# Performance work log

Measured on AMD Instinct MI355X. Metric: run time of the kernel, lower is better.

Reference implementation:

```python
import jax, jax.numpy as jnp
import numpy as np

D_MODEL, D_STATE, D_CONV, EXPAND = 1024, 16, 4, 2
D_INNER = EXPAND * D_MODEL
DT_RANK = D_MODEL // 16
B, T = 2, 4096
EPS = 1e-5


def setup_inputs() -> dict:
    key = jax.random.key(0)
    ks = jax.random.split(key, 8)
    s = lambda k, shape, sc: jax.random.normal(k, shape, jnp.float32) * sc
    return {
        "x": s(ks[0], (B, T, D_MODEL), 1.0),
        "norm_w": jnp.ones((D_MODEL,), jnp.float32),
        "w_in": s(ks[1], (D_MODEL, 2 * D_INNER), 0.02),
        "conv_w": s(ks[2], (D_INNER, 1, D_CONV), 0.1),   # depthwise kernel (O,I/g,K)
        "conv_b": jnp.zeros((D_INNER,), jnp.float32),
        "w_x": s(ks[3], (D_INNER, DT_RANK + 2 * D_STATE), 0.02),
        "w_dt": s(ks[4], (DT_RANK, D_INNER), 0.02),
        "b_dt": s(ks[5], (D_INNER,), 0.02),
        "A_log": jnp.log(jnp.broadcast_to(
            jnp.arange(1, D_STATE + 1, dtype=jnp.float32), (D_INNER, D_STATE))),
        "D": jnp.ones((D_INNER,), jnp.float32),
        "w_out": s(ks[6], (D_INNER, D_MODEL), 0.02),
    }


def _rmsnorm(x, w):
    return x * jax.lax.rsqrt(jnp.mean(x * x, axis=-1, keepdims=True) + EPS) * w


def _mamba(x, w_in, conv_w, conv_b, w_x, w_dt, b_dt, A_log, Dp, w_out):
    xr = x @ w_in                                  # (B,T,2*D_INNER)
    u, res = jnp.split(xr, 2, axis=-1)
    # causal depthwise conv over time
    uc = jnp.transpose(u, (0, 2, 1))               # (B,D_INNER,T)
    uc = jax.lax.conv_general_dilated(
        uc, conv_w, window_strides=(1,), padding=[(D_CONV - 1, 0)],
        dimension_numbers=("NCH", "OIH", "NCH"), feature_group_count=D_INNER)
    u = jax.nn.silu(jnp.transpose(uc, (0, 2, 1)) + conv_b)  # (B,T,D_INNER)

    xdbc = u @ w_x                                 # (B,T,DT_RANK+2*D_STATE)
    dt, Bm, Cm = jnp.split(xdbc, [DT_RANK, DT_RANK + D_STATE], axis=-1)
    delta = jax.nn.softplus(dt @ w_dt + b_dt)      # (B,T,D_INNER)
    A = -jnp.exp(A_log)                            # (D_INNER,D_STATE)

    def step(h, inp):
        d_t, b_t, c_t, u_t = inp                   # (B,Di),(B,N),(B,N),(B,Di)
        dA = jnp.exp(d_t[:, :, None] * A)          # (B,Di,N)
        h = dA * h + (d_t * u_t)[:, :, None] * b_t[:, None, :]
        y_t = jnp.einsum("bdn,bn->bd", h, c_t)
        return h, y_t

    h0 = jnp.zeros((x.shape[0], D_INNER, D_STATE), x.dtype)
    xs = (jnp.swapaxes(delta, 0, 1), jnp.swapaxes(Bm, 0, 1),
          jnp.swapaxes(Cm, 0, 1), jnp.swapaxes(u, 0, 1))
    _, ys = jax.lax.scan(step, h0, xs)             # ys: (T,B,D_INNER)
    y = jnp.swapaxes(ys, 0, 1) + u * Dp            # (B,T,D_INNER)
    y = y * jax.nn.silu(res)
    return y @ w_out                               # (B,T,D_MODEL)


def reference(x, norm_w, w_in, conv_w, conv_b, w_x, w_dt, b_dt, A_log, D, w_out):
    return x + _mamba(_rmsnorm(x, norm_w), w_in, conv_w, conv_b,
                      w_x, w_dt, b_dt, A_log, D, w_out)
```

## Files before the change

### kernel.cpp

```cpp
#include <hip/hip_runtime.h>
#include <hip/hip_bf16.h>
#include <cmath>

typedef __hip_bfloat16 bf16;
typedef __attribute__((ext_vector_type(8))) short short8;
typedef __attribute__((ext_vector_type(4))) short short4v;
typedef __attribute__((ext_vector_type(4))) float floatx4;
typedef __attribute__((ext_vector_type(2))) float floatx2;
typedef __attribute__((ext_vector_type(4))) int intx4;

#define DMODEL 1024
#define DSTATE 16
#define DINNER 2048
#define DTRANK 64
#define NB 2
#define NT 4096
#define NM (NB * NT)
#define GG (2 * DINNER)
#define CL 64
#define NC (NT / CL)
#define LOG2E 1.4426950408889634f

typedef __attribute__((address_space(1))) const void gvoid;
typedef __attribute__((address_space(3))) void lvoid;
static __device__ __forceinline__ void gl_lds16(const bf16* g, bf16* l) {
  __builtin_amdgcn_global_load_lds((gvoid*)g, (lvoid*)l, 16, 0, 0);
}
static __device__ __forceinline__ void gl_lds16b(const void* g, void* l) {
  __builtin_amdgcn_global_load_lds((gvoid*)g, (lvoid*)l, 16, 0, 0);
}

static __device__ __forceinline__ float bits2f(unsigned short s) {
  unsigned u = ((unsigned)s) << 16;
  float f;
  __builtin_memcpy(&f, &u, 4);
  return f;
}
static __device__ __forceinline__ short f2bits(float f) {
  bf16 h = __float2bfloat16(f);
  short s;
  __builtin_memcpy(&s, &h, 2);
  return s;
}

__global__ void detect_k(const void* __restrict__ a_log_raw, int* __restrict__ flag,
                         int* __restrict__ sflag) {
  int lane = threadIdx.x;
  unsigned first = ((const unsigned*)a_log_raw)[0];
  int fl = (first != 0u) ? 1 : 0;
  int n = lane & 15;
  int grp = lane >> 4;
  int dsel = (grp == 0) ? 0 : (grp == 1) ? 1 : (grp == 2) ? 777 : 2047;
  int idx = dsel * DSTATE + n;
  float v = fl ? bits2f(((const unsigned short*)a_log_raw)[idx])
               : ((const float*)a_log_raw)[idx];
  float a = __expf(v);
  float tgt = (float)(n + 1);
  bool ok2 = fabsf(a - tgt) < 1e-5f * tgt;
  bool ok1 = fabsf(a - tgt) < 1.5e-2f * tgt;
  unsigned long long m2 = __ballot(ok2);
  unsigned long long m1 = __ballot(ok1);
  if (lane == 0) {
    *flag = fl;
    *sflag = (m2 == ~0ull) ? 2 : (m1 == ~0ull) ? 1 : 0;
  }
}

static __device__ __forceinline__ bf16 cvt1(const void* in, int i, int fl) {
  return fl ? ((const bf16*)in)[i] : __float2bfloat16(((const float*)in)[i]);
}
__global__ void convert_small_k(
    const void* nw, const void* cw, const void* cb, const void* bdt,
    const void* al, const void* dp, bf16* nwb, bf16* cwb, bf16* cbb, bf16* bdtb,
    bf16* alogb, bf16* Db, const int* __restrict__ flag) {
  int i = blockIdx.x * 256 + threadIdx.x;
  int fl = *flag;
  if (i < 1024) { nwb[i] = cvt1(nw, i, fl); return; } i -= 1024;
  if (i < 8192) { cwb[i] = cvt1(cw, i, fl); return; } i -= 8192;
  if (i < 2048) { cbb[i] = cvt1(cb, i, fl); return; } i -= 2048;
  if (i < 2048) { bdtb[i] = cvt1(bdt, i, fl); return; } i -= 2048;
  if (i < 32768) { alogb[i] = cvt1(al, i, fl); return; } i -= 32768;
  if (i < 2048) { Db[i] = cvt1(dp, i, fl); }
}

__global__ void transpose_k(const void* __restrict__ in, bf16* __restrict__ out,
                            int R, int C, const int* __restrict__ flag) {
  size_t idx = (size_t)blockIdx.x * 256 + threadIdx.x;
  if (idx >= (size_t)R * C) return;
  int fl = *flag;
  int c = (int)(idx / R);
  int r = (int)(idx % R);
  size_t src = (size_t)r * C + c;
  bf16 v = fl ? ((const bf16*)in)[src] : __float2bfloat16(((const float*)in)[src]);
  out[(size_t)c * R + r] = v;
}

__global__ __launch_bounds__(256) void transpose_tile_k(
    const void* __restrict__ in, bf16* __restrict__ out, int R, int C,
    const int* __restrict__ flag) {
  __shared__ bf16 t[64][65];
  int c0 = blockIdx.x * 64, r0 = blockIdx.y * 64;
  int fl = *flag;
  int ci = threadIdx.x & 63, grp = threadIdx.x >> 6;
#pragma unroll
  for (int rr = grp; rr < 64; rr += 4) {
    size_t src = (size_t)(r0 + rr) * C + c0 + ci;
    t[rr][ci] = fl ? ((const bf16*)in)[src]
                   : __float2bfloat16(((const float*)in)[src]);
  }
  __syncthreads();
#pragma unroll
  for (int cc = grp; cc < 64; cc += 4) {
    out[(size_t)(c0 + cc) * R + r0 + ci] = t[ci][cc];
  }
}

__global__ __launch_bounds__(256) void rmsnorm_k(const void* __restrict__ x,
                                                 const bf16* __restrict__ w,
                                                 bf16* __restrict__ xn,
                                                 const int* __restrict__ flag) {
  int row = blockIdx.x;
  int tid = threadIdx.x;
  int fl = *flag;
  float f[4];
  if (fl) {
    short4v raw = *(const short4v*)((const bf16*)x + (size_t)row * DMODEL + tid * 4);
#pragma unroll
    for (int k = 0; k < 4; k++) f[k] = bits2f((unsigned short)raw[k]);
  } else {
    floatx4 raw = *(const floatx4*)((const float*)x + (size_t)row * DMODEL + tid * 4);
#pragma unroll
    for (int k = 0; k < 4; k++) f[k] = raw[k];
  }
  float s = f[0] * f[0] + f[1] * f[1] + f[2] * f[2] + f[3] * f[3];
#pragma unroll
  for (int o = 32; o > 0; o >>= 1) s += __shfl_down(s, o);
  __shared__ float ps[4];
  __shared__ float stot;
  if ((tid & 63) == 0) ps[tid >> 6] = s;
  __syncthreads();
  if (tid == 0) stot = ps[0] + ps[1] + ps[2] + ps[3];
  __syncthreads();
  float scale = 1.0f / sqrtf(stot * (1.0f / DMODEL) + 1e-5f);
  short4v wr = *(const short4v*)(w + tid * 4);
  short4v o;
#pragma unroll
  for (int k = 0; k < 4; k++)
    o[k] = f2bits(f[k] * scale * bits2f((unsigned short)wr[k]));
  *(short4v*)(xn + (size_t)row * DMODEL + tid * 4) = o;
}

template <int EPI, int MT>
__global__ __launch_bounds__(256, 2) void gemm_bt(
    const bf16* __restrict__ A, const bf16* __restrict__ Bt, void* __restrict__ Cout,
    int M, int N, int K, int Ks, const bf16* __restrict__ eb,
    const void* __restrict__ ex, bf16* __restrict__ dtb,
    const int* __restrict__ flag) {
  constexpr int AI = MT / 32;
  constexpr bool COEPI = (EPI == 0 || EPI == 2 || EPI == 3 || EPI == 5);
  constexpr int AB_BYTES = (MT * 32 + 128 * 32) * 2;
  constexpr int ET_BYTES = COEPI ? 32 * 132 * 4 : 0;
  constexpr int SM_BYTES = AB_BYTES > ET_BYTES ? AB_BYTES : ET_BYTES;
  __shared__ __align__(16) char smraw[SM_BYTES];
  bf16* As = (bf16*)smraw;
  bf16* Bs = (bf16*)smraw + MT * 32;
  float* ET = (float*)smraw;

  int tid = threadIdx.x;
  int lane = tid & 63;
  int wave = tid >> 6;
  int wm = (wave >> 1) * (MT / 2), wn = (wave & 1) * 64;
  int m0 = blockIdx.y * MT, n0 = blockIdx.x * 128;
  int koff = (EPI == 4) ? blockIdx.z * K : 0;

  floatx4 acc[AI][4] = {};

  int sr = tid >> 2;
  int sc = (tid & 3) * 8;
  int bn0 = n0 + sr;        if (bn0 > N - 1) bn0 = N - 1;
  int bn1 = n0 + sr + 64;   if (bn1 > N - 1) bn1 = N - 1;
  bf16* asb = As + wave * 512;
  bf16* bsb = Bs + wave * 512;

  const bf16* a0p = A + (size_t)(m0 + sr) * Ks + sc + koff;
  const bf16* a1p = A + (size_t)(m0 + sr + (MT == 128 ? 64 : 0)) * Ks + sc + koff;
  const bf16* b0p = Bt + (size_t)bn0 * Ks + sc + koff;
  const bf16* b1p = Bt + (size_t)bn1 * Ks + sc + koff;

  for (int k0 = 0; k0 < K; k0 += 32) {
    __syncthreads();
    gl_lds16(a0p + k0, asb);
    if (MT == 128) gl_lds16(a1p + k0, asb + 64 * 32);
    gl_lds16(b0p + k0, bsb);
    gl_lds16(b1p + k0, bsb + 64 * 32);
    __syncthreads();

    int fr = lane & 15;
    int q = lane >> 4;
    short8 af[AI], bfr[4];
#pragma unroll
    for (int i = 0; i < AI; i++)
      af[i] = *(const short8*)(As + (wm + i * 16 + fr) * 32 + q * 8);
#pragma unroll
    for (int j = 0; j < 4; j++)
      bfr[j] = *(const short8*)(Bs + (wn + j * 16 + fr) * 32 + q * 8);
#pragma unroll
    for (int i = 0; i < AI; i++)
#pragma unroll
      for (int j = 0; j < 4; j++)
        acc[i][j] =
            __builtin_amdgcn_mfma_f32_16x16x32_bf16(af[i], bfr[j], acc[i][j], 0, 0, 0);
  }

  int cr = (lane >> 4) * 4;
  int cc = lane & 15;

  if constexpr (COEPI) {
    int fl = (EPI == 3) ? *flag : 0;
    bool sil = (EPI == 5) && (n0 >= DINNER);
    int lrb = (wave >> 1) * 16 + cr;
    int r2 = tid >> 3;
#pragma unroll
    for (int i = 0; i < AI; i++) {
      __syncthreads();
#pragma unroll
      for (int j = 0; j < 4; j++)
#pragma unroll
        for (int r = 0; r < 4; r++)
          ET[(lrb + r) * 132 + wn + j * 16 + cc] = acc[i][j][r];
      __syncthreads();
      int m = m0 + i * 16 + (r2 < 16 ? r2 : r2 + 48);
      size_t rowo = (size_t)m * N + n0;
      if constexpr (EPI == 0 || EPI == 5) {
#pragma unroll
        for (int c = 0; c < 2; c++) {
          int col = (tid & 7) * 8 + c * 64;
          floatx4 f0 = *(const floatx4*)&ET[r2 * 132 + col];
          floatx4 f1 = *(const floatx4*)&ET[r2 * 132 + col + 4];
          short8 o8;
#pragma unroll
          for (int k = 0; k < 4; k++) {
            float v0 = f0[k], v1 = f1[k];
            if (EPI == 5 && sil) {
              v0 = v0 / (1.f + __expf(-v0));
              v1 = v1 / (1.f + __expf(-v1));
            }
            o8[k] = f2bits(v0);
            o8[4 + k] = f2bits(v1);
          }
          *(short8*)((bf16*)Cout + rowo + col) = o8;
        }
      } else if constexpr (EPI == 2) {
#pragma unroll
        for (int c = 0; c < 4; c++) {
          int col = (tid & 7) * 4 + c * 32;
          floatx4 f = *(const floatx4*)&ET[r2 * 132 + col];
          short4v eb4 = *(const short4v*)(eb + n0 + col);
          floatx4 o;
#pragma unroll
          for (int k = 0; k < 4; k++) {
            float t = f[k] + bits2f((unsigned short)eb4[k]);
            o[k] = (t > 15.f) ? t : __logf(1.f + __expf(t));
          }
          *(floatx4*)((float*)Cout + rowo + col) = o;
        }
      } else {
#pragma unroll
        for (int c = 0; c < 4; c++) {
          int col = (tid & 7) * 4 + c * 32;
          floatx4 f = *(const floatx4*)&ET[r2 * 132 + col];
          if (fl) {
            short4v xv = *(const short4v*)((const bf16*)ex + rowo + col);
            short4v o;
#pragma unroll
            for (int k = 0; k < 4; k++)
              o[k] = f2bits(f[k] + bits2f((unsigned short)xv[k]));
            *(short4v*)((bf16*)Cout + rowo + col) = o;
          } else {
            floatx4 xv = *(const floatx4*)((const float*)ex + rowo + col);
            floatx4 o;
#pragma unroll
            for (int k = 0; k < 4; k++) o[k] = f[k] + xv[k];
            *(floatx4*)((float*)Cout + rowo + col) = o;
          }
        }
      }
    }
  } else {
#pragma unroll
    for (int i = 0; i < AI; i++) {
#pragma unroll
      for (int j = 0; j < 4; j++) {
        int n = n0 + wn + j * 16 + cc;
        if (n >= N) continue;
#pragma unroll
        for (int r = 0; r < 4; r++) {
          int m = m0 + wm + i * 16 + cr + r;
          float v = acc[i][j][r];
          size_t o = (size_t)m * N + n;
          if (EPI == 1) {
            ((float*)Cout)[o] = v;
            if (n < DTRANK) dtb[(size_t)m * DTRANK + n] = __float2bfloat16(v);
          } else {
            ((float*)Cout)[((size_t)blockIdx.z * M + m) * N + n] = v;
          }
        }
      }
    }
  }
}

__global__ void reduce_dt_k(const float* __restrict__ part, float* __restrict__ xdbc,
                            bf16* __restrict__ dtb) {
  int idx = blockIdx.x * 256 + threadIdx.x;
  const int seg = NM * 96;
  float s = part[idx] + part[seg + idx] + part[2 * seg + idx] + part[3 * seg + idx];
  xdbc[idx] = s;
  int m = idx / 96, n = idx - m * 96;
  if (n < DTRANK) dtb[m * DTRANK + n] = __float2bfloat16(s);
}

__global__ __launch_bounds__(256) void conv_silu_k(const bf16* __restrict__ xr,
                                                   const bf16* __restrict__ cw,
                                                   const bf16* __restrict__ cb,
                                                   bf16* __restrict__ u) {
  size_t i8 = ((size_t)blockIdx.x * 256 + threadIdx.x) * 8;
  int col = (int)(i8 & (DINNER - 1));
  size_t m = i8 >> 11;
  int t = (int)(m & (NT - 1));
  float wv[8][4];
  {
    short8 w01 = *(const short8*)(cw + col * 4);
    short8 w23 = *(const short8*)(cw + col * 4 + 8);
    short8 w45 = *(const short8*)(cw + col * 4 + 16);
    short8 w67 = *(const short8*)(cw + col * 4 + 24);
#pragma unroll
    for (int j = 0; j < 4; j++) {
      wv[0][j] = bits2f((unsigned short)w01[j]);
      wv[1][j] = bits2f((unsigned short)w01[4 + j]);
      wv[2][j] = bits2f((unsigned short)w23[j]);
      wv[3][j] = bits2f((unsigned short)w23[4 + j]);
      wv[4][j] = bits2f((unsigned short)w45[j]);
      wv[5][j] = bits2f((unsigned short)w45[4 + j]);
      wv[6][j] = bits2f((unsigned short)w67[j]);
      wv[7][j] = bits2f((unsigned short)w67[4 + j]);
    }
  }
  short8 bias = *(const short8*)(cb + col);
  short8 rows[4] = {};
  const bf16* baseT = xr + m * GG + col;
  if (t >= 3) {
#pragma unroll
    for (int j = 0; j < 4; j++)
      rows[j] = *(const short8*)(baseT + (ptrdiff_t)(j - 3) * GG);
  } else {
    for (int j = 3 - t; j < 4; j++)
      rows[j] = *(const short8*)(baseT + (ptrdiff_t)(j - 3) * GG);
  }
  short8 outv;
#pragma unroll
  for (int i = 0; i < 8; i++) {
    float acc = bits2f((unsigned short)bias[i]);
#pragma unroll
    for (int j = 0; j < 4; j++)
      acc = fmaf(wv[i][j], bits2f((unsigned short)rows[j][i]), acc);
    float s = acc / (1.f + __expf(-acc));
    outv[i] = f2bits(s);
  }
  *(short8*)(u + m * DINNER + col) = outv;
}


template <int SM>
static __device__ __forceinline__ void scan1_impl(
    float* __restrict__ smB,
    const float* __restrict__ delta, const bf16* __restrict__ u,
    const float* __restrict__ xdbc, const bf16* __restrict__ A_log,
    float* __restrict__ chunkSd, float* __restrict__ chunkS) {
  int tid = threadIdx.x;
  int bc = blockIdx.x;
  int dblk = bc & 7;
  int chunk = (bc >> 3) & (NC - 1);
  int b = bc >> 9;
  int d = (dblk << 8) + tid;
  size_t base = (size_t)b * NT + (size_t)chunk * CL;

  {
    int byte = tid * 16;
    int t = byte >> 6;
    gl_lds16b((const char*)xdbc + (base + t) * 384 + 256 + (byte & 63),
              (char*)smB + byte);
  }

  const floatx2 one2 = {1.f, 1.f};
  float AvL[16];
  floatx2 rc2[8];
  if (SM == 0) {
#pragma unroll
    for (int k = 0; k < 16; k++)
      AvL[k] = -__expf((float)A_log[d * DSTATE + k]) * LOG2E;
  } else if (SM == 1) {
#pragma unroll
    for (int p = 0; p < 8; p++) {
      rc2[p][0] = __expf((float)A_log[d * DSTATE + 2 * p]) - (float)(2 * p + 1);
      rc2[p][1] = __expf((float)A_log[d * DSTATE + 2 * p + 1]) - (float)(2 * p + 2);
    }
  }

  const float* pd = delta + base * DINNER + d;
  const bf16* pu = u + base * DINNER + d;

  floatx2 h2[8] = {};
  float sd = 0.f;

  auto body = [&](float dlc, float uuc, int t) {
    float du = dlc * uuc;
    sd += dlc;
    floatx2 du2 = {du, du};
    const floatx4* bq = (const floatx4*)&smB[t * 16];
    floatx4 b0 = bq[0], b1 = bq[1], b2 = bq[2], b3 = bq[3];
    floatx2 B2[8] = {{b0[0], b0[1]}, {b0[2], b0[3]}, {b1[0], b1[1]}, {b1[2], b1[3]},
                     {b2[0], b2[1]}, {b2[2], b2[3]}, {b3[0], b3[1]}, {b3[2], b3[3]}};
    if (SM >= 1) {
      float e0 = exp2f(dlc * -LOG2E);
      float e2 = e0 * e0;
      floatx2 dv = {e0, e2};
      floatx2 e2v = {e2, e2};
      floatx2 mdl2 = {-dlc, -dlc};
#pragma unroll
      for (int p = 0; p < 8; p++) {
        floatx2 cA2 = dv;
        if (SM == 1)
          cA2 = dv * __builtin_elementwise_fma(mdl2, rc2[p], one2);
        h2[p] = __builtin_elementwise_fma(cA2, h2[p], du2 * B2[p]);
        dv *= e2v;
      }
    } else {
#pragma unroll
      for (int p = 0; p < 8; p++) {
        floatx2 cA2 = {exp2f(dlc * AvL[2 * p]), exp2f(dlc * AvL[2 * p + 1])};
        h2[p] = __builtin_elementwise_fma(cA2, h2[p], du2 * B2[p]);
      }
    }
  };

  float dlA = *pd, uuA = (float)*pu;
  pd += DINNER; pu += DINNER;
  __syncthreads();
  float dlB, uuB;
  for (int t = 0; t + 2 < CL; t += 2) {
    dlB = *pd; uuB = (float)*pu;
    pd += DINNER; pu += DINNER;
    body(dlA, uuA, t);
    dlA = *pd; uuA = (float)*pu;
    pd += DINNER; pu += DINNER;
    body(dlB, uuB, t + 1);
  }
  dlB = *pd; uuB = (float)*pu;
  body(dlA, uuA, CL - 2);
  body(dlB, uuB, CL - 1);

  size_t cidx = ((size_t)b * NC + chunk) * DINNER + d;
  float* out = chunkS + cidx * DSTATE;
  floatx4 S0 = {h2[0][0], h2[0][1], h2[1][0], h2[1][1]};
  floatx4 S1 = {h2[2][0], h2[2][1], h2[3][0], h2[3][1]};
  floatx4 S2 = {h2[4][0], h2[4][1], h2[5][0], h2[5][1]};
  floatx4 S3 = {h2[6][0], h2[6][1], h2[7][0], h2[7][1]};
  *(floatx4*)(out) = S0;
  *(floatx4*)(out + 4) = S1;
  *(floatx4*)(out + 8) = S2;
  *(floatx4*)(out + 12) = S3;
  chunkSd[cidx] = sd;
}

__global__ __launch_bounds__(256) void scan1_k(
    const float* __restrict__ delta, const bf16* __restrict__ u,
    const float* __restrict__ xdbc, const bf16* __restrict__ A_log,
    float* __restrict__ chunkSd, float* __restrict__ chunkS,
    const int* __restrict__ sflag) {
  __shared__ float smB[CL * 16];
  int sm = *sflag;
  if (sm == 2)      scan1_impl<2>(smB, delta, u, xdbc, A_log, chunkSd, chunkS);
  else if (sm == 1) scan1_impl<1>(smB, delta, u, xdbc, A_log, chunkSd, chunkS);
  else              scan1_impl<0>(smB, delta, u, xdbc, A_log, chunkSd, chunkS);
}

__global__ __launch_bounds__(256) void scan2_k(
    const float* __restrict__ chunkSd, const float* __restrict__ chunkS,
    const bf16* __restrict__ A_log, float* __restrict__ chunkH) {
  int tid = threadIdx.x;
  int bc = blockIdx.x;
  int dblk = bc & 31;
  int b = bc >> 5;
  int d = (dblk << 6) + (tid >> 2);
  int n0 = (tid & 3) * 4;
  float AvL[4];
#pragma unroll
  for (int k = 0; k < 4; k++)
    AvL[k] = -__expf((float)A_log[d * DSTATE + n0 + k]) * LOG2E;
  floatx4 h = {};
  size_t c0 = (size_t)b * NC * DINNER + d;
  size_t o0 = c0 * DSTATE + n0;
  floatx4 S = *(const floatx4*)(chunkS + o0);
  float sd = chunkSd[c0];
  for (int c = 0; c < NC; c++) {
    floatx4 Sn = {};
    float sd_n = 0.f;
    if (c + 1 < NC) {
      size_t cn = c0 + (size_t)(c + 1) * DINNER;
      Sn = *(const floatx4*)(chunkS + cn * DSTATE + n0);
      sd_n = chunkSd[cn];
    }
    size_t o = o0 + (size_t)c * DINNER * DSTATE;
    *(floatx4*)(chunkH + o) = h;
#pragma unroll
    for (int k = 0; k < 4; k++) h[k] = fmaf(exp2f(AvL[k] * sd), h[k], S[k]);
    S = Sn; sd = sd_n;
  }
}

template <int SM>
static __device__ __forceinline__ void scan3_impl(
    float* __restrict__ smBC,
    const float* __restrict__ delta, const bf16* __restrict__ u,
    const float* __restrict__ xdbc, const bf16* __restrict__ xr,
    const bf16* __restrict__ A_log, const bf16* __restrict__ Dp,
    const float* __restrict__ chunkH, bf16* __restrict__ y) {
  int tid = threadIdx.x;
  int bc = blockIdx.x;
  int dblk = bc & 7;
  int chunk = (bc >> 3) & (NC - 1);
  int b = bc >> 9;
  int d = (dblk << 8) + tid;
  size_t base = (size_t)b * NT + (size_t)chunk * CL;

#pragma unroll
  for (int j = 0; j < 2; j++) {
    int byte = (tid + 256 * j) * 16;
    int t = byte >> 7;
    gl_lds16b((const char*)xdbc + (base + t) * 384 + 256 + (byte & 127),
              (char*)smBC + byte);
  }

  const floatx2 one2 = {1.f, 1.f};
  float AvL[16];
  floatx2 rc2[8];
  if (SM == 0) {
#pragma unroll
    for (int k = 0; k < 16; k++)
      AvL[k] = -__expf((float)A_log[d * DSTATE + k]) * LOG2E;
  } else if (SM == 1) {
#pragma unroll
    for (int p = 0; p < 8; p++) {
      rc2[p][0] = __expf((float)A_log[d * DSTATE + 2 * p]) - (float)(2 * p + 1);
      rc2[p][1] = __expf((float)A_log[d * DSTATE + 2 * p + 1]) - (float)(2 * p + 2);
    }
  }
  float Dd = (float)Dp[d];
  floatx2 h2[8];
  {
    const float* hp = chunkH + (((size_t)b * NC + chunk) * DINNER + d) * DSTATE;
    floatx4 H0 = *(const floatx4*)(hp);
    floatx4 H1 = *(const floatx4*)(hp + 4);
    floatx4 H2 = *(const floatx4*)(hp + 8);
    floatx4 H3 = *(const floatx4*)(hp + 12);
    h2[0] = {H0[0], H0[1]}; h2[1] = {H0[2], H0[3]};
    h2[2] = {H1[0], H1[1]}; h2[3] = {H1[2], H1[3]};
    h2[4] = {H2[0], H2[1]}; h2[5] = {H2[2], H2[3]};
    h2[6] = {H3[0], H3[1]}; h2[7] = {H3[2], H3[3]};
  }

  const float* pd = delta + base * DINNER + d;
  const bf16* pu = u + base * DINNER + d;
  const bf16* pg = xr + base * GG + DINNER + d;
  bf16* py = y + base * DINNER + d;

  auto body = [&](float dlc, float uuc, float gfc, int t) {
    float du = dlc * uuc;
    floatx2 du2 = {du, du};
    const floatx4* bq = (const floatx4*)&smBC[t * 32];
    floatx4 b0 = bq[0], b1 = bq[1], b2 = bq[2], b3 = bq[3];
    floatx4 c0 = bq[4], c1 = bq[5], c2 = bq[6], c3 = bq[7];
    floatx2 B2[8] = {{b0[0], b0[1]}, {b0[2], b0[3]}, {b1[0], b1[1]}, {b1[2], b1[3]},
                     {b2[0], b2[1]}, {b2[2], b2[3]}, {b3[0], b3[1]}, {b3[2], b3[3]}};
    floatx2 C2[8] = {{c0[0], c0[1]}, {c0[2], c0[3]}, {c1[0], c1[1]}, {c1[2], c1[3]},
                     {c2[0], c2[1]}, {c2[2], c2[3]}, {c3[0], c3[1]}, {c3[2], c3[3]}};
    floatx2 ys2 = {0.f, 0.f};
    if (SM >= 1) {
      float e0 = exp2f(dlc * -LOG2E);
      float e2 = e0 * e0;
      floatx2 dv = {e0, e2};
      floatx2 e2v = {e2, e2};
      floatx2 mdl2 = {-dlc, -dlc};
#pragma unroll
      for (int p = 0; p < 8; p++) {
        floatx2 cA2 = dv;
        if (SM == 1)
          cA2 = dv * __builtin_elementwise_fma(mdl2, rc2[p], one2);
        h2[p] = __builtin_elementwise_fma(cA2, h2[p], du2 * B2[p]);
        ys2 = __builtin_elementwise_fma(h2[p], C2[p], ys2);
        dv *= e2v;
      }
    } else {
#pragma unroll
      for (int p = 0; p < 8; p++) {
        floatx2 cA2 = {exp2f(dlc * AvL[2 * p]), exp2f(dlc * AvL[2 * p + 1])};
        h2[p] = __builtin_elementwise_fma(cA2, h2[p], du2 * B2[p]);
        ys2 = __builtin_elementwise_fma(h2[p], C2[p], ys2);
      }
    }
    float ys = ys2[0] + ys2[1];
    *py = __float2bfloat16((ys + uuc * Dd) * gfc);
    py += DINNER;
  };

  float dlA = *pd, uuA = (float)*pu, gfA = (float)*pg;
  pd += DINNER; pu += DINNER; pg += GG;
  __syncthreads();
  float dlB, uuB, gfB;
  for (int t = 0; t + 2 < CL; t += 2) {
    dlB = *pd; uuB = (float)*pu; gfB = (float)*pg;
    pd += DINNER; pu += DINNER; pg += GG;
    body(dlA, uuA, gfA, t);
    dlA = *pd; uuA = (float)*pu; gfA = (float)*pg;
    pd += DINNER; pu += DINNER; pg += GG;
    body(dlB, uuB, gfB, t + 1);
  }
  dlB = *pd; uuB = (float)*pu; gfB = (float)*pg;
  body(dlA, uuA, gfA, CL - 2);
  body(dlB, uuB, gfB, CL - 1);
}

__global__ __launch_bounds__(256) void scan3_k(
    const float* __restrict__ delta, const bf16* __restrict__ u,
    const float* __restrict__ xdbc, const bf16* __restrict__ xr,
    const bf16* __restrict__ A_log, const bf16* __restrict__ Dp,
    const float* __restrict__ chunkH, bf16* __restrict__ y,
    const int* __restrict__ sflag) {
  __shared__ float smBC[CL * 32];
  int sm = *sflag;
  if (sm == 2)      scan3_impl<2>(smBC, delta, u, xdbc, xr, A_log, Dp, chunkH, y);
  else if (sm == 1) scan3_impl<1>(smBC, delta, u, xdbc, xr, A_log, Dp, chunkH, y);
  else              scan3_impl<0>(smBC, delta, u, xdbc, xr, A_log, Dp, chunkH, y);
}

extern "C" void kernel_launch(void* const* d_in, const int* in_sizes, int n_in,
                              void* d_out, int out_size, void* d_ws, size_t ws_size,
                              hipStream_t stream) {
  const void* x_raw = d_in[0];
  const void* norm_w_raw = d_in[1];
  const void* w_in_raw = d_in[2];
  const void* conv_w_raw = d_in[3];
  const void* conv_b_raw = d_in[4];
  const void* w_x_raw = d_in[5];
  const void* w_dt_raw = d_in[6];
  const void* b_dt_raw = d_in[7];
  const void* A_log_raw = d_in[8];
  const void* Dp_raw = d_in[9];
  const void* w_out_raw = d_in[10];

  char* ws = (char*)d_ws;
  size_t off = 0;
  auto alloc = [&](size_t bytes) {
    size_t o = off;
    off += (bytes + 255) & ~(size_t)255;
    return o;
  };
  int* flag = (int*)(ws + alloc(256));
  int* sflag = flag + 64;
  bf16* nwb = (bf16*)(ws + alloc((size_t)DMODEL * 2));
  bf16* cwb = (bf16*)(ws + alloc((size_t)DINNER * 4 * 2));
  bf16* cbb = (bf16*)(ws + alloc((size_t)DINNER * 2));
  bf16* bdtb = (bf16*)(ws + alloc((size_t)DINNER * 2));
  bf16* alogb = (bf16*)(ws + alloc((size_t)DINNER * DSTATE * 2));
  bf16* Db = (bf16*)(ws + alloc((size_t)DINNER * 2));
  bf16* xn = (bf16*)(ws + alloc((size_t)NM * DMODEL * 2));
  bf16* xr = (bf16*)(ws + alloc((size_t)NM * GG * 2));
  bf16* u = (bf16*)(ws + alloc((size_t)NM * DINNER * 2));
  float* xdbc = (float*)(ws + alloc((size_t)NM * 96 * 4));
  bf16* dtb = (bf16*)(ws + alloc((size_t)NM * 64 * 2));
  float* delta = (float*)(ws + alloc((size_t)NM * DINNER * 4));
  bf16* yb = (bf16*)(ws + alloc((size_t)NM * DINNER * 2));
  bf16* w_inT = (bf16*)(ws + alloc((size_t)DMODEL * GG * 2));
  bf16* w_xT = (bf16*)(ws + alloc((size_t)DINNER * 96 * 2));
  bf16* w_dtT = (bf16*)(ws + alloc((size_t)DTRANK * DINNER * 2));
  bf16* w_outT = (bf16*)(ws + alloc((size_t)DINNER * DMODEL * 2));
  float* chunkS = (float*)xn;
  float* chunkH = (float*)(ws + alloc((size_t)NB * NC * DINNER * DSTATE * 4));
  float* chunkSd = (float*)(ws + alloc((size_t)NB * NC * DINNER * 4));
  float* part = delta;

  detect_k<<<1, 64, 0, stream>>>(A_log_raw, flag, sflag);

  convert_small_k<<<(48128 + 255) / 256, 256, 0, stream>>>(
      norm_w_raw, conv_w_raw, conv_b_raw, b_dt_raw, A_log_raw, Dp_raw,
      nwb, cwb, cbb, bdtb, alogb, Db, flag);

  transpose_tile_k<<<dim3(GG / 64, DMODEL / 64), 256, 0, stream>>>(w_in_raw, w_inT, DMODEL, GG, flag);
  transpose_k<<<(DINNER * 96 + 255) / 256, 256, 0, stream>>>(w_x_raw, w_xT, DINNER, 96, flag);
  transpose_tile_k<<<dim3(DINNER / 64, DTRANK / 64), 256, 0, stream>>>(w_dt_raw, w_dtT, DTRANK, DINNER, flag);
  transpose_tile_k<<<dim3(DMODEL / 64, DINNER / 64), 256, 0, stream>>>(w_out_raw, w_outT, DINNER, DMODEL, flag);

  rmsnorm_k<<<NM, 256, 0, stream>>>(x_raw, nwb, xn, flag);

  gemm_bt<5, 128><<<dim3(GG / 128, NM / 128), 256, 0, stream>>>(
      xn, w_inT, xr, NM, GG, DMODEL, DMODEL, nullptr, nullptr, nullptr, flag);

  conv_silu_k<<<(size_t)NM * DINNER / 8 / 256, 256, 0, stream>>>(xr, cwb, cbb, u);

  gemm_bt<4, 64><<<dim3(1, NM / 64, 4), 256, 0, stream>>>(
      u, w_xT, part, NM, 96, DINNER / 4, DINNER, nullptr, nullptr, nullptr, flag);
  reduce_dt_k<<<NM * 96 / 256, 256, 0, stream>>>(part, xdbc, dtb);

  gemm_bt<2, 128><<<dim3(DINNER / 128, NM / 128), 256, 0, stream>>>(
      dtb, w_dtT, delta, NM, DINNER, DTRANK, DTRANK, bdtb, nullptr, nullptr, flag);

  scan1_k<<<NB * NC * 8, 256, 0, stream>>>(delta, u, xdbc, alogb, chunkSd, chunkS, sflag);
  scan2_k<<<NB * 32, 256, 0, stream>>>(chunkSd, chunkS, alogb, chunkH);
  scan3_k<<<NB * NC * 8, 256, 0, stream>>>(delta, u, xdbc, xr, alogb, Db, chunkH, yb, sflag);

  gemm_bt<3, 128><<<dim3(DMODEL / 128, NM / 128), 256, 0, stream>>>(
      yb, w_outT, d_out, NM, DMODEL, DINNER, DINNER, nullptr, x_raw, nullptr, flag);
}
```

Measured before the change: 528.5 us.

## Double GEMM K-tile to 64 with XOR-swizzled LDS layout

The bf16 MFMA GEMM now stages a 64-wide K slice of A and B into LDS per iteration instead of 32. Each thread's 16-byte chunk is placed by an XOR swizzle on the column index, so fragment reads avoid LDS bank conflicts. This halves the number of barrier pairs and load rounds per K, but doubles LDS use per block, which may reduce occupancy. The epilogue row mapping now depends on MT, so tile sizes other than 128 write to the correct rows.

```diff
diff --git a/kernel.cpp b/kernel.cpp
--- a/kernel.cpp
+++ b/kernel.cpp
@@ -158,12 +158,12 @@
     const int* __restrict__ flag) {
   constexpr int AI = MT / 32;
   constexpr bool COEPI = (EPI == 0 || EPI == 2 || EPI == 3 || EPI == 5);
-  constexpr int AB_BYTES = (MT * 32 + 128 * 32) * 2;
+  constexpr int AB_BYTES = (MT * 64 + 128 * 64) * 2;
   constexpr int ET_BYTES = COEPI ? 32 * 132 * 4 : 0;
   constexpr int SM_BYTES = AB_BYTES > ET_BYTES ? AB_BYTES : ET_BYTES;
   __shared__ __align__(16) char smraw[SM_BYTES];
   bf16* As = (bf16*)smraw;
-  bf16* Bs = (bf16*)smraw + MT * 32;
+  bf16* Bs = (bf16*)smraw + MT * 64;
   float* ET = (float*)smraw;
 
   int tid = threadIdx.x;
@@ -175,41 +175,58 @@
 
   floatx4 acc[AI][4] = {};
 
-  int sr = tid >> 2;
-  int sc = (tid & 3) * 8;
-  int bn0 = n0 + sr;        if (bn0 > N - 1) bn0 = N - 1;
-  int bn1 = n0 + sr + 64;   if (bn1 > N - 1) bn1 = N - 1;
-  bf16* asb = As + wave * 512;
-  bf16* bsb = Bs + wave * 512;
-
-  const bf16* a0p = A + (size_t)(m0 + sr) * Ks + sc + koff;
-  const bf16* a1p = A + (size_t)(m0 + sr + (MT == 128 ? 64 : 0)) * Ks + sc + koff;
-  const bf16* b0p = Bt + (size_t)bn0 * Ks + sc + koff;
-  const bf16* b1p = Bt + (size_t)bn1 * Ks + sc + koff;
-
-  for (int k0 = 0; k0 < K; k0 += 32) {
+  int rc = wave * 8 + (lane >> 3);
+  int cb = ((lane & 7) ^ (lane >> 3)) * 8;
+  const bf16* ap = A + (size_t)(m0 + rc) * Ks + cb + koff;
+  const bf16* bp0;
+  const bf16* bp1;
+  const bf16* bp2;
+  const bf16* bp3;
+  {
+    int e0 = n0 + rc;        if (e0 > N - 1) e0 = N - 1;
+    int e1 = n0 + 32 + rc;   if (e1 > N - 1) e1 = N - 1;
+    int e2 = n0 + 64 + rc;   if (e2 > N - 1) e2 = N - 1;
+    int e3 = n0 + 96 + rc;   if (e3 > N - 1) e3 = N - 1;
+    bp0 = Bt + (size_t)e0 * Ks + cb + koff;
+    bp1 = Bt + (size_t)e1 * Ks + cb + koff;
+    bp2 = Bt + (size_t)e2 * Ks + cb + koff;
+    bp3 = Bt + (size_t)e3 * Ks + cb + koff;
+  }
+  bf16* asw = As + wave * 8 * 64;
+  bf16* bsw = Bs + wave * 8 * 64;
+
+  int fr = lane & 15;
+  int q = lane >> 4;
+  int sw8 = fr & 7;
+
+  for (int k0 = 0; k0 < K; k0 += 64) {
     __syncthreads();
-    gl_lds16(a0p + k0, asb);
-    if (MT == 128) gl_lds16(a1p + k0, asb + 64 * 32);
-    gl_lds16(b0p + k0, bsb);
-    gl_lds16(b1p + k0, bsb + 64 * 32);
+#pragma unroll
+    for (int c = 0; c < MT / 32; c++)
+      gl_lds16(ap + (size_t)c * 32 * Ks + k0, asw + c * 32 * 64);
+    gl_lds16(bp0 + k0, bsw);
+    gl_lds16(bp1 + k0, bsw + 32 * 64);
+    gl_lds16(bp2 + k0, bsw + 64 * 64);
+    gl_lds16(bp3 + k0, bsw + 96 * 64);
     __syncthreads();
 
-    int fr = lane & 15;
-    int q = lane >> 4;
-    short8 af[AI], bfr[4];
-#pragma unroll
-    for (int i = 0; i < AI; i++)
-      af[i] = *(const short8*)(As + (wm + i * 16 + fr) * 32 + q * 8);
-#pragma unroll
-    for (int j = 0; j < 4; j++)
-      bfr[j] = *(const short8*)(Bs + (wn + j * 16 + fr) * 32 + q * 8);
-#pragma unroll
-    for (int i = 0; i < AI; i++)
+#pragma unroll
+    for (int kk = 0; kk < 2; kk++) {
+      int bb = ((kk * 4 + q) ^ sw8) * 8;
+      short8 af[AI], bfr[4];
+#pragma unroll
+      for (int i = 0; i < AI; i++)
+        af[i] = *(const short8*)(As + (wm + i * 16 + fr) * 64 + bb);
 #pragma unroll
       for (int j = 0; j < 4; j++)
-        acc[i][j] =
-            __builtin_amdgcn_mfma_f32_16x16x32_bf16(af[i], bfr[j], acc[i][j], 0, 0, 0);
+        bfr[j] = *(const short8*)(Bs + (wn + j * 16 + fr) * 64 + bb);
+#pragma unroll
+      for (int i = 0; i < AI; i++)
+#pragma unroll
+        for (int j = 0; j < 4; j++)
+          acc[i][j] = __builtin_amdgcn_mfma_f32_16x16x32_bf16(af[i], bfr[j],
+                                                              acc[i][j], 0, 0, 0);
+    }
   }
 
   int cr = (lane >> 4) * 4;
@@ -229,7 +246,7 @@
         for (int r = 0; r < 4; r++)
           ET[(lrb + r) * 132 + wn + j * 16 + cc] = acc[i][j][r];
       __syncthreads();
-      int m = m0 + i * 16 + (r2 < 16 ? r2 : r2 + 48);
+      int m = m0 + i * 16 + (r2 < 16 ? r2 : r2 + (MT / 2 - 16));
       size_t rowo = (size_t)m * N + n0;
       if constexpr (EPI == 0 || EPI == 5) {
 #pragma unroll
```

Measured after the change: 540.6 us. 2.3% more time.
